# Kernel tuning notes

Hardware: AMD Instinct MI355X
Metric: run time of the kernel (lower is better)

## Reference

```python
import jax, jax.numpy as jnp
import numpy as np

C_IN = 3072
C_OUT = 1024
MAJ = 3  # majority_size


def setup_inputs() -> dict:
    key = jax.random.key(0)
    k1, k2 = jax.random.split(key)
    x = jax.random.normal(k1, (256, C_IN), dtype=jnp.float32)
    stdv = 1.0 / np.sqrt(C_OUT * C_IN)
    weight = jax.random.uniform(k2, (C_OUT, C_IN), dtype=jnp.float32, minval=-stdv, maxval=stdv)
    return {"input": x, "weight": weight}


def reference(input, weight):
    B = input.shape[0]
    G = C_IN // MAJ  # number of majority groups
    # Deterministic binarization (sign), as in Binarize(..., 'det')
    xb = jnp.sign(input)            # [B, C_IN]
    wb = jnp.sign(weight)           # [C_OUT, C_IN]
    # Grouped products: inter[b,c,g] = sum_k xb[b,g,k] * wb[c,g,k]
    # (equivalent to einsum('bj,cj->bcj') followed by reshape+sum over groups of 3)
    xg = xb.reshape(B, G, MAJ)
    wg = wb.reshape(C_OUT, G, MAJ)
    inter = jnp.einsum('bgk,cgk->bcg', xg, wg)  # [B, C_OUT, G]
    # Majority vote: clamp group sums to [-1, 1], sum across groups, scale by 2.25
    out = jnp.sum(jnp.clip(inter, -1.0, 1.0), axis=2) * 2.25  # [B, C_OUT]
    return out
```

## Files before the change

kernel.cpp:

```cpp
#include <hip/hip_runtime.h>
#include <stdint.h>


#define B_SZ  256
#define C_IN  3072
#define C_OUT 1024
#define CHUNKS_W 4096
#define CHUNKS_TOT 5120


__global__ __launch_bounds__(256) void pack_signs(const float* __restrict__ x,
                                                  const float* __restrict__ w,
                                                  uint64_t* __restrict__ wpk,
                                                  uint64_t* __restrict__ xpk) {
    int wave = blockIdx.x * 4 + (threadIdx.x >> 6);
    int lane = threadIdx.x & 63;
#pragma unroll
    for (int i = 0; i < 5; ++i) {
        int ch = wave * 5 + i;
        const float* src;
        uint64_t* dst;
        if (ch < CHUNKS_W) {
            int c = ch >> 2, q = ch & 3;
            src = w + (size_t)c * C_IN + q * 768;
            dst = wpk + ((size_t)q * C_OUT + c) * 12;
        } else {
            int id = ch - CHUNKS_W;
            int b = id >> 2, q = id & 3;
            src = x + (size_t)b * C_IN + q * 768;
            dst = xpk + ((size_t)b * 4 + q) * 12;
        }
        const float4* s4 = (const float4*)(src + 12 * lane);
        float4 f0 = s4[0], f1 = s4[1], f2 = s4[2];
        float v[12] = {f0.x, f0.y, f0.z, f0.w,
                       f1.x, f1.y, f1.z, f1.w,
                       f2.x, f2.y, f2.z, f2.w};
        uint64_t pl[12];
#pragma unroll
        for (int m = 0; m < 12; ++m)
            pl[m] = __ballot(v[m] > 0.0f);
        if (lane == 0) {
#pragma unroll
            for (int m = 0; m < 12; ++m)
                dst[m] = pl[m];
        }
    }
}

__global__ __launch_bounds__(256) void maj_main(const uint64_t* __restrict__ wpk,
                                                const uint64_t* __restrict__ xpk,
                                                float* __restrict__ out) {
    int tid = threadIdx.x;
    int blk = blockIdx.x;
    int b0  = (blk >> 2) * 2;
    int c   = (blk & 3) * 256 + tid;

    int acc0 = 0, acc1 = 0;
#pragma unroll
    for (int q = 0; q < 4; ++q) {
        const uint64_t* wb = wpk + ((size_t)q * C_OUT + c) * 12;
        const uint64_t* x0 = xpk + ((size_t)(b0 + 0) * 4 + q) * 12;
        const uint64_t* x1 = xpk + ((size_t)(b0 + 1) * 4 + q) * 12;
        uint64_t Wv[12];
#pragma unroll
        for (int m = 0; m < 12; ++m) Wv[m] = wb[m];
#pragma unroll
        for (int j = 0; j < 4; ++j) {
            uint64_t t0 = x0[3 * j + 0] ^ Wv[3 * j + 0];
            uint64_t t1 = x0[3 * j + 1] ^ Wv[3 * j + 1];
            uint64_t t2 = x0[3 * j + 2] ^ Wv[3 * j + 2];
            acc0 += __popcll((t0 & t1) | (t2 & (t0 | t1)));
            uint64_t u0 = x1[3 * j + 0] ^ Wv[3 * j + 0];
            uint64_t u1 = x1[3 * j + 1] ^ Wv[3 * j + 1];
            uint64_t u2 = x1[3 * j + 2] ^ Wv[3 * j + 2];
            acc1 += __popcll((u0 & u1) | (u2 & (u0 | u1)));
        }
    }
    out[(size_t)(b0 + 0) * C_OUT + c] = 2304.0f - 4.5f * (float)acc0;
    out[(size_t)(b0 + 1) * C_OUT + c] = 2304.0f - 4.5f * (float)acc1;
}

extern "C" void kernel_launch(void* const* d_in, const int* in_sizes, int n_in,
                              void* d_out, int out_size, void* d_ws, size_t ws_size,
                              hipStream_t stream) {
    const float* x = (const float*)d_in[0];
    const float* w = (const float*)d_in[1];
    float* out = (float*)d_out;

    uint64_t* wpk = (uint64_t*)d_ws;
    uint64_t* xpk = (uint64_t*)((char*)d_ws + 393216);

    pack_signs<<<256, 256, 0, stream>>>(x, w, wpk, xpk);
    maj_main<<<512, 256, 0, stream>>>(wpk, xpk, out);
}
```

Before: 70.76 us.

## Fuse input sign packing into main kernel via shared memory

Moves packing of the input signs out of the pack kernel and into the main kernel. Each block now packs its own two rows into shared memory, after a __syncthreads. The weight pack kernel becomes one chunk per wave over 1024 blocks instead of five chunks per wave over 256, which spreads the work across more blocks. Each x row is repacked by the 4 blocks that share it, so some input pack work is redundant, in exchange for removing the xpk global round trip and simplifying the pack stage.

```diff
diff --git a/kernel.cpp b/kernel.cpp
--- a/kernel.cpp
+++ b/kernel.cpp
@@ -2,68 +2,70 @@
 #include <stdint.h>
 
 
-#define B_SZ  256
 #define C_IN  3072
 #define C_OUT 1024
-#define CHUNKS_W 4096
-#define CHUNKS_TOT 5120
 
+__global__ __launch_bounds__(256) void pack_w(const float* __restrict__ w,
+                                              uint64_t* __restrict__ wpk) {
+    int j    = blockIdx.x * 4 + (threadIdx.x >> 6);
+    int lane = threadIdx.x & 63;
+    int c = j >> 2, q = j & 3;
+    const float* src = w + (size_t)c * C_IN + q * 768;
+    const float4* s4 = (const float4*)(src + 12 * lane);
+    float4 f0 = s4[0], f1 = s4[1], f2 = s4[2];
+    float v[12] = {f0.x, f0.y, f0.z, f0.w,
+                   f1.x, f1.y, f1.z, f1.w,
+                   f2.x, f2.y, f2.z, f2.w};
+    uint64_t pl[12];
+#pragma unroll
+    for (int m = 0; m < 12; ++m)
+        pl[m] = __ballot(v[m] > 0.0f);
+    if (lane == 0) {
+        uint64_t* dst = wpk + ((size_t)q * C_OUT + c) * 12;
+#pragma unroll
+        for (int m = 0; m < 12; ++m)
+            dst[m] = pl[m];
+    }
+}
 
-__global__ __launch_bounds__(256) void pack_signs(const float* __restrict__ x,
-                                                  const float* __restrict__ w,
-                                                  uint64_t* __restrict__ wpk,
-                                                  uint64_t* __restrict__ xpk) {
-    int wave = blockIdx.x * 4 + (threadIdx.x >> 6);
-    int lane = threadIdx.x & 63;
+__global__ __launch_bounds__(256) void maj_main(const float* __restrict__ x,
+                                                const uint64_t* __restrict__ wpk,
+                                                float* __restrict__ out) {
+    __shared__ uint64_t xs[96];
+    int tid  = threadIdx.x;
+    int lane = tid & 63;
+    int wv   = tid >> 6;
+    int blk  = blockIdx.x;
+    int b0   = (blk >> 2) * 2;
+    int c    = (blk & 3) * 256 + tid;
+
 #pragma unroll
-    for (int i = 0; i < 5; ++i) {
-        int ch = wave * 5 + i;
-        const float* src;
-        uint64_t* dst;
-        if (ch < CHUNKS_W) {
-            int c = ch >> 2, q = ch & 3;
-            src = w + (size_t)c * C_IN + q * 768;
-            dst = wpk + ((size_t)q * C_OUT + c) * 12;
-        } else {
-            int id = ch - CHUNKS_W;
-            int b = id >> 2, q = id & 3;
-            src = x + (size_t)b * C_IN + q * 768;
-            dst = xpk + ((size_t)b * 4 + q) * 12;
-        }
+    for (int i = 0; i < 2; ++i) {
+        int job = wv * 2 + i;
+        int bi = job >> 2, q = job & 3;
+        const float* src = x + (size_t)(b0 + bi) * C_IN + q * 768;
         const float4* s4 = (const float4*)(src + 12 * lane);
         float4 f0 = s4[0], f1 = s4[1], f2 = s4[2];
         float v[12] = {f0.x, f0.y, f0.z, f0.w,
                        f1.x, f1.y, f1.z, f1.w,
                        f2.x, f2.y, f2.z, f2.w};
-        uint64_t pl[12];
 #pragma unroll
-        for (int m = 0; m < 12; ++m)
-            pl[m] = __ballot(v[m] > 0.0f);
-        if (lane == 0) {
-#pragma unroll
-            for (int m = 0; m < 12; ++m)
-                dst[m] = pl[m];
+        for (int m = 0; m < 12; ++m) {
+            uint64_t pl = __ballot(v[m] > 0.0f);
+            if (lane == 0) xs[job * 12 + m] = pl;
         }
     }
-}
-
-__global__ __launch_bounds__(256) void maj_main(const uint64_t* __restrict__ wpk,
-                                                const uint64_t* __restrict__ xpk,
-                                                float* __restrict__ out) {
-    int tid = threadIdx.x;
-    int blk = blockIdx.x;
-    int b0  = (blk >> 2) * 2;
-    int c   = (blk & 3) * 256 + tid;
+    __syncthreads();
 
     int acc0 = 0, acc1 = 0;
 #pragma unroll
     for (int q = 0; q < 4; ++q) {
         const uint64_t* wb = wpk + ((size_t)q * C_OUT + c) * 12;
-        const uint64_t* x0 = xpk + ((size_t)(b0 + 0) * 4 + q) * 12;
-        const uint64_t* x1 = xpk + ((size_t)(b0 + 1) * 4 + q) * 12;
         uint64_t Wv[12];
 #pragma unroll
         for (int m = 0; m < 12; ++m) Wv[m] = wb[m];
+        const uint64_t* x0 = &xs[(0 * 4 + q) * 12];
+        const uint64_t* x1 = &xs[(1 * 4 + q) * 12];
 #pragma unroll
         for (int j = 0; j < 4; ++j) {
             uint64_t t0 = x0[3 * j + 0] ^ Wv[3 * j + 0];
@@ -88,8 +90,7 @@
     float* out = (float*)d_out;
 
     uint64_t* wpk = (uint64_t*)d_ws;
-    uint64_t* xpk = (uint64_t*)((char*)d_ws + 393216);
 
-    pack_signs<<<256, 256, 0, stream>>>(x, w, wpk, xpk);
-    maj_main<<<512, 256, 0, stream>>>(wpk, xpk, out);
+    pack_w<<<1024, 256, 0, stream>>>(w, wpk);
+    maj_main<<<512, 256, 0, stream>>>(x, wpk, out);
 }
```

Measured after the change: 71.64 us. No clear change (+1.2%).
